# Optimization experiments

Hardware: AMD Instinct MI355X
Metric: run time of the kernel (lower is better)

Reference implementation:

```python
import jax, jax.numpy as jnp
import numpy as np

B, T, C, H = 128, 256, 256, 8
HS = C // H  # 32
EPS = 1e-5


def _layernorm(x, g, b):
    mu = jnp.mean(x, axis=-1, keepdims=True)
    var = jnp.mean(jnp.square(x - mu), axis=-1, keepdims=True)
    return g * (x - mu) / jnp.sqrt(var + EPS) + b


def setup_inputs() -> dict:
    key = jax.random.key(0)
    ks = jax.random.split(key, 12)
    s = 0.02
    return {
        "x": jax.random.normal(ks[0], (B, T, C), dtype=jnp.float32),
        "Wk": jax.random.normal(ks[1], (H, C, HS), dtype=jnp.float32) * s,
        "Wq": jax.random.normal(ks[2], (H, C, HS), dtype=jnp.float32) * s,
        "Wv": jax.random.normal(ks[3], (H, C, HS), dtype=jnp.float32) * s,
        "Wp": jax.random.normal(ks[4], (C, C), dtype=jnp.float32) * s,
        "bp": jnp.zeros((C,), dtype=jnp.float32),
        "W1": jax.random.normal(ks[5], (C, 4 * C), dtype=jnp.float32) * s,
        "b1": jnp.zeros((4 * C,), dtype=jnp.float32),
        "W2": jax.random.normal(ks[6], (4 * C, C), dtype=jnp.float32) * s,
        "b2": jnp.zeros((C,), dtype=jnp.float32),
        "g1": jnp.ones((C,), dtype=jnp.float32),
        "be1": jnp.zeros((C,), dtype=jnp.float32),
        "g2": jnp.ones((C,), dtype=jnp.float32),
        "be2": jnp.zeros((C,), dtype=jnp.float32),
    }


def reference(x, Wk, Wq, Wv, Wp, bp, W1, b1, W2, b2, g1, be1, g2, be2):
    Bx, Tx, Cx = x.shape
    # --- multi-head self-attention on ln1(x) ---
    h = _layernorm(x, g1, be1)
    k = jnp.einsum('btc,hcd->bhtd', h, Wk)
    q = jnp.einsum('btc,hcd->bhtd', h, Wq)
    v = jnp.einsum('btc,hcd->bhtd', h, Wv)
    # NOTE: source computes k @ q^T (transposed vs standard) and scales by C**-0.5
    scores = jnp.einsum('bhtd,bhsd->bhts', k, q) * (Cx ** -0.5)
    mask = jnp.tril(jnp.ones((Tx, Tx), dtype=bool))  # causal lower-triangular
    scores = jnp.where(mask, scores, -jnp.inf)
    w = jax.nn.softmax(scores, axis=-1)
    o = jnp.einsum('bhts,bhsd->bhtd', w, v)
    o = o.transpose(0, 2, 1, 3).reshape(Bx, Tx, Cx)  # concat heads
    x = x + (o @ Wp + bp)
    # --- feed-forward (swish) on ln2(x) ---
    h2 = _layernorm(x, g2, be2)
    f = h2 @ W1 + b1
    f = f * jax.nn.sigmoid(f)  # swish
    f = f @ W2 + b2
    return x + f
```

## Files before the change

kernel.cpp:

```cpp
#include <hip/hip_runtime.h>
#include <cstdint>

#define BB 128
#define TT 256
#define CC 256
#define HH 8
#define HSZ 32
#define NT (BB*TT)
#define CF (4*CC)
#define LN_EPS 1e-5f
#define SCALE 0.0625f

typedef __attribute__((ext_vector_type(8))) __bf16 bf16x8;
typedef __attribute__((ext_vector_type(4))) float f32x4;
typedef __attribute__((ext_vector_type(16))) float f32x16;
typedef __attribute__((ext_vector_type(2))) long i64x2;
typedef unsigned short u16;
typedef unsigned int u32;
typedef unsigned char u8;

__device__ __forceinline__ u16 f2bf(float f) {
  u32 u = __float_as_uint(f);
  u32 r = (u + 0x7fffu + ((u >> 16) & 1u)) >> 16;
  return (u16)r;
}
__device__ __forceinline__ u8 f2f8(float f) {
  return (u8)(__builtin_amdgcn_cvt_pk_fp8_f32(f, f, 0, false) & 0xff);
}
__device__ __forceinline__ u32 f2f8x4(float a, float b, float c, float d) {
  u32 pk = (u32)__builtin_amdgcn_cvt_pk_fp8_f32(a, b, 0, false);
  return (u32)__builtin_amdgcn_cvt_pk_fp8_f32(c, d, (int)pk, true);
}
__device__ __forceinline__ uint2 f2bfx4(float a, float b, float c, float d) {
  uint2 r;
  asm("v_cvt_pk_bf16_f32 %0, %1, %2" : "=v"(r.x) : "v"(a), "v"(b));
  asm("v_cvt_pk_bf16_f32 %0, %1, %2" : "=v"(r.y) : "v"(c), "v"(d));
  return r;
}
__device__ __forceinline__ int swz3i(int r) { return (r ^ (r >> 2)) & 3; }
__device__ __forceinline__ int pkrow(int row, int k) {
  int g = (k >> 4) & 3, h = (k >> 3) & 1, j = k & 7;
  int c = (h << 1) + (g >> 1);
  int cp = c ^ swz3i(row);
  return (k & ~63) + cp * 16 + ((g & 1) << 3) + j;
}

__device__ __forceinline__ void gload16(const void* g, void* l) {
  __builtin_amdgcn_global_load_lds(
      (const __attribute__((address_space(1))) u32*)(uintptr_t)g,
      (__attribute__((address_space(3))) u32*)(u32)(uintptr_t)l,
      16, 0, 0);
}

__device__ __forceinline__ void wait_vm0() {
  asm volatile("s_waitcnt vmcnt(0)" ::: "memory");
  __builtin_amdgcn_sched_barrier(0);
}
__device__ __forceinline__ void wait_vm4() {
  asm volatile("s_waitcnt vmcnt(4)" ::: "memory");
  __builtin_amdgcn_sched_barrier(0);
}
__device__ __forceinline__ void wait_vm8() {
  asm volatile("s_waitcnt vmcnt(8)" ::: "memory");
  __builtin_amdgcn_sched_barrier(0);
}
__device__ __forceinline__ void wait_vm4_lgkm0() {
  asm volatile("s_waitcnt vmcnt(4) lgkmcnt(0)" ::: "memory");
  __builtin_amdgcn_sched_barrier(0);
}
__device__ __forceinline__ void wait_vm0_lgkm0() {
  asm volatile("s_waitcnt vmcnt(0) lgkmcnt(0)" ::: "memory");
  __builtin_amdgcn_sched_barrier(0);
}
__device__ __forceinline__ void sbar() {
  __builtin_amdgcn_s_barrier();
  __builtin_amdgcn_sched_barrier(0);
}

__global__ __launch_bounds__(256) void conv_t(
    const float* __restrict__ Wk, const float* __restrict__ Wq,
    const float* __restrict__ Wv, const float* __restrict__ Wp,
    const float* __restrict__ W1, const float* __restrict__ W2,
    u8* __restrict__ WkqvT8, u8* __restrict__ WpT8,
    u8* __restrict__ W1T8, u8* __restrict__ W2T8) {
  __shared__ u8 ldsT[64][68];
  int bid = blockIdx.x, tid = threadIdx.x;
  int n0, k0, K;
  u8* dst;
  int mode;
  const float* src = nullptr;
  int sk = 0;
  if (bid < 48) {
    mode = 0; n0 = (bid >> 2) * 64; k0 = (bid & 3) * 64; K = 256; dst = WkqvT8;
  } else if (bid < 112) {
    int l = bid - 48;
    mode = 1; n0 = (l >> 2) * 64; k0 = (l & 3) * 64; K = 256; dst = W1T8;
    src = W1; sk = 1024;
  } else if (bid < 176) {
    int l = bid - 112;
    mode = 1; n0 = (l >> 4) * 64; k0 = (l & 15) * 64; K = 1024; dst = W2T8;
    src = W2; sk = 256;
  } else {
    int l = bid - 176;
    mode = 1; n0 = (l >> 2) * 64; k0 = (l & 3) * 64; K = 256; dst = WpT8;
    src = Wp; sk = 256;
  }
  int kr = tid >> 2;
  int nbase = (tid & 3) * 16;
#pragma unroll
  for (int u = 0; u < 4; ++u) {
    int nl = nbase + u * 4;
    int ng = n0 + nl;
    float4 v;
    if (mode == 0) {
      const float* W = (ng < 256) ? Wk : (ng < 512 ? Wq : Wv);
      int inner = ng & 255;
      v = *reinterpret_cast<const float4*>(
          &W[((inner >> 5) << 13) + (size_t)(k0 + kr) * 32 + (inner & 31)]);
    } else {
      v = *reinterpret_cast<const float4*>(
          &src[(size_t)(k0 + kr) * sk + ng]);
    }
    ldsT[nl + 0][kr] = f2f8(v.x);
    ldsT[nl + 1][kr] = f2f8(v.y);
    ldsT[nl + 2][kr] = f2f8(v.z);
    ldsT[nl + 3][kr] = f2f8(v.w);
  }
  __syncthreads();
  int nl = tid >> 2;
  int nglob = n0 + nl;
  int sz = swz3i(nglob);
  u8* drow = dst + (size_t)nglob * K + k0;
#pragma unroll
  for (int c4 = (tid & 3) * 4; c4 < (tid & 3) * 4 + 4; ++c4) {
    int q = c4 >> 1, s = c4 & 1;
    int kb = q * 8 + s * 4;
    u32 pk = (u32)ldsT[nl][kb] | ((u32)ldsT[nl][kb + 1] << 8) |
             ((u32)ldsT[nl][kb + 2] << 16) | ((u32)ldsT[nl][kb + 3] << 24);
    int g = (kb >> 4) & 3, h8 = (kb >> 3) & 1;
    int cp = ((h8 << 1) + (g >> 1)) ^ sz;
    *reinterpret_cast<u32*>(drow + cp * 16 + ((g & 1) << 3) + (kb & 7)) = pk;
  }
}

__global__ __launch_bounds__(256) void ln_kernel(const float* __restrict__ x,
                                                 const float* __restrict__ g,
                                                 const float* __restrict__ b,
                                                 u8* __restrict__ out) {
  int tid = threadIdx.x;
  int wid = tid >> 6, lane = tid & 63;
  int row = blockIdx.x * 4 + wid;
  const float4 v = reinterpret_cast<const float4*>(x + (size_t)row * CC)[lane];
  float s = v.x + v.y + v.z + v.w;
#pragma unroll
  for (int o = 32; o; o >>= 1) s += __shfl_xor(s, o, 64);
  float mu = s * (1.0f / CC);
  float dx = v.x - mu, dy = v.y - mu, dz = v.z - mu, dw = v.w - mu;
  float ss = dx * dx + dy * dy + dz * dz + dw * dw;
#pragma unroll
  for (int o = 32; o; o >>= 1) ss += __shfl_xor(ss, o, 64);
  float inv = rsqrtf(ss * (1.0f / CC) + LN_EPS);
  const float4 gv = reinterpret_cast<const float4*>(g)[lane];
  const float4 bv = reinterpret_cast<const float4*>(b)[lane];
  u32 pk = f2f8x4(gv.x * dx * inv + bv.x, gv.y * dy * inv + bv.y,
                  gv.z * dz * inv + bv.z, gv.w * dw * inv + bv.w);
  *reinterpret_cast<u32*>(out + (size_t)row * CC + pkrow(row, lane * 4)) = pk;
}

template <int EPI>
__device__ __forceinline__ void epi_store(f32x4 v, int m, int n,
                                          const float* bias,
                                          const float* resid, void* outp,
                                          int N) {
  size_t off = (size_t)m * N + n;
  if (EPI == 0) {
    u16 pk[4];
#pragma unroll
    for (int r = 0; r < 4; ++r) pk[r] = f2bf(v[r]);
    *reinterpret_cast<uint2*>(&((u16*)outp)[off]) = *reinterpret_cast<uint2*>(pk);
  } else if (EPI == 1) {
    const float4 bv = *reinterpret_cast<const float4*>(&bias[n]);
    const float4 rv = *reinterpret_cast<const float4*>(&resid[off]);
    float4 o;
    o.x = v[0] + bv.x + rv.x;
    o.y = v[1] + bv.y + rv.y;
    o.z = v[2] + bv.z + rv.z;
    o.w = v[3] + bv.w + rv.w;
    *reinterpret_cast<float4*>(&((float*)outp)[off]) = o;
  }
}

template <int NB, int EPI>
__global__ __launch_bounds__(512, 4) void panel_fused(
    const u8* __restrict__ Asrc, const u8* __restrict__ WT8,
    const float* __restrict__ bias, const float* __restrict__ resid,
    void* __restrict__ outp, int N,
    const float* __restrict__ gamma, const float* __restrict__ beta,
    u8* __restrict__ out8) {
  __shared__ u8 Bw[4][256][64];
  __shared__ float red[4][64][2];
  int tid = threadIdx.x;
  int w = tid >> 6, lane = tid & 63;
  int l32 = lane & 31, h = lane >> 5;
  int th = w >> 2, fq = w & 3;
  int m0 = blockIdx.x * 64;

#define STAGEP(nb)                                                            \
  {                                                                           \
    _Pragma("unroll") for (int it = 0; it < 8; ++it) {                        \
      int f = it * 512 + tid;                                                 \
      int kg = f >> 10, t = (f >> 2) & 255, c = f & 3;                        \
      gload16(WT8 + (size_t)((nb) * 256 + t) * 256 + kg * 64 + c * 16,        \
              &Bw[0][0][0] + f * 16);                                         \
    }                                                                         \
  }
  i64x2 aa[4][2];
  {
    int ar = th * 32 + l32;
    int az = swz3i(ar);
#pragma unroll
    for (int kg = 0; kg < 4; ++kg)
#pragma unroll
      for (int p = 0; p < 2; ++p)
        aa[kg][p] = *reinterpret_cast<const i64x2*>(
            Asrc + (size_t)(m0 + ar) * 256 + kg * 64 +
            ((((h << 1) + p) ^ az) << 4));
  }
  STAGEP(0);

#pragma unroll 1
  for (int nb = 0; nb < NB; ++nb) {
    if (nb == 0) wait_vm0(); else wait_vm8();
    sbar();
    f32x16 a1[2] = {};
#pragma unroll
    for (int kg = 0; kg < 4; ++kg) {
#pragma unroll
      for (int p = 0; p < 2; ++p) {
        i64x2 bB[2];
#pragma unroll
        for (int j = 0; j < 2; ++j) {
          int br = fq * 64 + j * 32 + l32, bz = swz3i(br);
          bB[j] = *reinterpret_cast<const i64x2*>(
              &Bw[kg][br][(((h << 1) + p) ^ bz) << 4]);
        }
#pragma unroll
        for (int j = 0; j < 2; ++j) {
          a1[j] = __builtin_amdgcn_mfma_f32_32x32x16_fp8_fp8(
              bB[j][0], aa[kg][p][0], a1[j], 0, 0, 0);
          a1[j] = __builtin_amdgcn_mfma_f32_32x32x16_fp8_fp8(
              bB[j][1], aa[kg][p][1], a1[j], 0, 0, 0);
        }
      }
    }
    sbar();
    if (nb < NB - 1) STAGEP(nb + 1);

    int m = m0 + th * 32 + l32;
    if (EPI == 2) {
      float s1 = 0.f, s2 = 0.f;
#pragma unroll
      for (int j = 0; j < 2; ++j) {
#pragma unroll
        for (int q = 0; q < 4; ++q) {
          int n = fq * 64 + j * 32 + q * 8 + h * 4;
          size_t off = (size_t)m * 256 + n;
          const float4 bv = *reinterpret_cast<const float4*>(&bias[n]);
          const float4 rv = *reinterpret_cast<const float4*>(&resid[off]);
          float4 o;
          o.x = a1[j][q * 4 + 0] + bv.x + rv.x;
          o.y = a1[j][q * 4 + 1] + bv.y + rv.y;
          o.z = a1[j][q * 4 + 2] + bv.z + rv.z;
          o.w = a1[j][q * 4 + 3] + bv.w + rv.w;
          *reinterpret_cast<float4*>(&((float*)outp)[off]) = o;
          a1[j][q * 4 + 0] = o.x; a1[j][q * 4 + 1] = o.y;
          a1[j][q * 4 + 2] = o.z; a1[j][q * 4 + 3] = o.w;
          s1 += (o.x + o.y) + (o.z + o.w);
          s2 += (o.x * o.x + o.y * o.y) + (o.z * o.z + o.w * o.w);
        }
      }
      s1 += __shfl_xor(s1, 32, 64);
      s2 += __shfl_xor(s2, 32, 64);
      if (h == 0) { red[fq][th * 32 + l32][0] = s1; red[fq][th * 32 + l32][1] = s2; }
      sbar();
      int tl = th * 32 + l32;
      float S1 = (red[0][tl][0] + red[1][tl][0]) + (red[2][tl][0] + red[3][tl][0]);
      float S2 = (red[0][tl][1] + red[1][tl][1]) + (red[2][tl][1] + red[3][tl][1]);
      float mu = S1 * (1.0f / 256.0f);
      float inv = rsqrtf(S2 * (1.0f / 256.0f) - mu * mu + LN_EPS);
#pragma unroll
      for (int j = 0; j < 2; ++j) {
#pragma unroll
        for (int q = 0; q < 4; ++q) {
          int n = fq * 64 + j * 32 + q * 8 + h * 4;
          const float4 gv = *reinterpret_cast<const float4*>(&gamma[n]);
          const float4 bb = *reinterpret_cast<const float4*>(&beta[n]);
          u32 pk = f2f8x4(gv.x * (a1[j][q * 4 + 0] - mu) * inv + bb.x,
                          gv.y * (a1[j][q * 4 + 1] - mu) * inv + bb.y,
                          gv.z * (a1[j][q * 4 + 2] - mu) * inv + bb.z,
                          gv.w * (a1[j][q * 4 + 3] - mu) * inv + bb.w);
          *reinterpret_cast<u32*>(out8 + (size_t)m * 256 + pkrow(m, n)) = pk;
        }
      }
    } else {
#pragma unroll
      for (int j = 0; j < 2; ++j) {
#pragma unroll
        for (int q = 0; q < 4; ++q) {
          int n = nb * 256 + fq * 64 + j * 32 + q * 8 + h * 4;
          f32x4 v = {a1[j][q * 4 + 0], a1[j][q * 4 + 1],
                     a1[j][q * 4 + 2], a1[j][q * 4 + 3]};
          epi_store<EPI>(v, m, n, bias, resid, outp, N);
        }
      }
    }
  }
#undef STAGEP
}

__global__ __launch_bounds__(512, 4) void ffn_fused(
    const u8* __restrict__ hb, const u8* __restrict__ W1T8,
    const u8* __restrict__ W2T8, const float* __restrict__ b1,
    const float* __restrict__ b2, const float* __restrict__ x2,
    float* __restrict__ outp) {
  __shared__ u8 Bw1[4][128][64];
  __shared__ u8 Bw2[2][256][64];
  __shared__ u8 Ff[2][64][64];
  __shared__ float b1l[1024];
  int tid = threadIdx.x;
  int w = tid >> 6, lane = tid & 63;
  int l32 = lane & 31, h = lane >> 5;
  int th = w >> 2, fq = w & 3;
  int m0 = blockIdx.x * 64;

#define STAGE_W1(nb)                                                          \
  {                                                                           \
    _Pragma("unroll") for (int it = 0; it < 4; ++it) {                        \
      int f = it * 512 + tid;                                                 \
      int kg = f >> 9, t = (f >> 2) & 127, c = f & 3;                         \
      gload16(W1T8 + (size_t)((nb) * 128 + t) * 256 + kg * 64 + c * 16,       \
              &Bw1[0][0][0] + f * 16);                                        \
    }                                                                         \
  }
#define STAGE_W2(nb)                                                          \
  {                                                                           \
    _Pragma("unroll") for (int it = 0; it < 4; ++it) {                        \
      int f = it * 512 + tid;                                                 \
      int kg2 = f >> 10, o = (f >> 2) & 255, c = f & 3;                       \
      gload16(W2T8 + (size_t)o * 1024 + (nb) * 128 + kg2 * 64 + c * 16,       \
              &Bw2[0][0][0] + f * 16);                                        \
    }                                                                         \
  }
  i64x2 aa[4][2];
  {
    int ar = th * 32 + l32;
    int az = swz3i(ar);
#pragma unroll
    for (int kg = 0; kg < 4; ++kg)
#pragma unroll
      for (int p = 0; p < 2; ++p)
        aa[kg][p] = *reinterpret_cast<const i64x2*>(
            hb + (size_t)(m0 + ar) * 256 + kg * 64 +
            ((((h << 1) + p) ^ az) << 4));
  }
  if (w < 4) gload16(b1 + (size_t)(w * 256 + lane * 4), b1l + w * 256 + lane * 4);
  STAGE_W1(0);
  STAGE_W2(0);

  f32x16 acc2[2] = {};
#pragma unroll 1
  for (int nb = 0; nb < 8; ++nb) {
    wait_vm4();
    sbar();
    f32x16 a1 = {};
#pragma unroll
    for (int kg = 0; kg < 4; ++kg) {
      int br = fq * 32 + l32, bz = swz3i(br);
#pragma unroll
      for (int p = 0; p < 2; ++p) {
        i64x2 bB = *reinterpret_cast<const i64x2*>(
            &Bw1[kg][br][(((h << 1) + p) ^ bz) << 4]);
        a1 = __builtin_amdgcn_mfma_f32_32x32x16_fp8_fp8(
            bB[0], aa[kg][p][0], a1, 0, 0, 0);
        a1 = __builtin_amdgcn_mfma_f32_32x32x16_fp8_fp8(
            bB[1], aa[kg][p][1], a1, 0, 0, 0);
      }
    }
    sbar();
    if (nb < 7) STAGE_W1(nb + 1);
    int kg2w = fq >> 1;
    {
      int t = th * 32 + l32;
      int tz = swz3i(t);
#pragma unroll
      for (int q = 0; q < 4; ++q) {
        int g = (fq & 1) * 2 + (q >> 1);
        int hh = q & 1;
        int c = (hh << 1) + (g >> 1);
        const float4 bv = *reinterpret_cast<const float4*>(
            &b1l[nb * 128 + fq * 32 + q * 8 + h * 4]);
        float bf[4] = {bv.x, bv.y, bv.z, bv.w};
        float sv[4];
#pragma unroll
        for (int r = 0; r < 4; ++r) {
          float fv = a1[q * 4 + r] + bf[r];
          float e = __builtin_amdgcn_exp2f(fv * -1.44269504f);
          sv[r] = fv * __builtin_amdgcn_rcpf(1.0f + e);
        }
        *reinterpret_cast<u32*>(
            &Ff[kg2w][t][((c ^ tz) << 4) + ((g & 1) << 3) + h * 4]) =
            f2f8x4(sv[0], sv[1], sv[2], sv[3]);
      }
    }
    if (nb < 7) wait_vm4_lgkm0();
    else        wait_vm0_lgkm0();
    sbar();
#pragma unroll
    for (int kg2 = 0; kg2 < 2; ++kg2)
#pragma unroll
      for (int p = 0; p < 2; ++p) {
        int ar2 = th * 32 + l32;
        i64x2 fa = *reinterpret_cast<const i64x2*>(
            &Ff[kg2][ar2][(((h << 1) + p) ^ swz3i(ar2)) << 4]);
        i64x2 bb2[2];
#pragma unroll
        for (int j = 0; j < 2; ++j) {
          int br = fq * 64 + j * 32 + l32;
          bb2[j] = *reinterpret_cast<const i64x2*>(
              &Bw2[kg2][br][(((h << 1) + p) ^ swz3i(br)) << 4]);
        }
#pragma unroll
        for (int j = 0; j < 2; ++j) {
          acc2[j] = __builtin_amdgcn_mfma_f32_32x32x16_fp8_fp8(
              bb2[j][0], fa[0], acc2[j], 0, 0, 0);
          acc2[j] = __builtin_amdgcn_mfma_f32_32x32x16_fp8_fp8(
              bb2[j][1], fa[1], acc2[j], 0, 0, 0);
        }
      }
    sbar();
    if (nb < 7) STAGE_W2(nb + 1);
  }
#undef STAGE_W1
#undef STAGE_W2
  int m = m0 + th * 32 + l32;
#pragma unroll
  for (int j = 0; j < 2; ++j) {
#pragma unroll
    for (int q = 0; q < 4; ++q) {
      int n = fq * 64 + j * 32 + q * 8 + h * 4;
      f32x4 v = {acc2[j][q * 4 + 0], acc2[j][q * 4 + 1],
                 acc2[j][q * 4 + 2], acc2[j][q * 4 + 3]};
      epi_store<1>(v, m, n, b2, x2, outp, CC);
    }
  }
}

__global__ __launch_bounds__(512) void attn_kernel(const u16* __restrict__ kqv,
                                                   u8* __restrict__ o8) {
  __shared__ u16 q_lds[256 * 32];
  __shared__ u16 vT[32 * 256];
  __shared__ u16 pT[8 * 16 * 64];
  int bh = blockIdx.x;
  int b = bh >> 3, h = bh & 7;
  int tid = threadIdx.x, wid = tid >> 6, lane = tid & 63;
  int l16 = lane & 15, lh = lane >> 4;
  const size_t rowbase = (size_t)b * TT * 768;
  {
    int sr = tid >> 2, c = tid & 3;
#pragma unroll
    for (int s = sr; s < 256; s += 128) {
      uint4 qv = *reinterpret_cast<const uint4*>(
          &kqv[rowbase + (size_t)s * 768 + 256 + h * 32 + c * 8]);
      *reinterpret_cast<uint4*>((char*)q_lds + ((s * 64 + c * 16) ^ ((s & 7) << 4))) = qv;
      u16 tmp[8];
      *reinterpret_cast<uint4*>(tmp) = *reinterpret_cast<const uint4*>(
          &kqv[rowbase + (size_t)s * 768 + 512 + h * 32 + c * 8]);
#pragma unroll
      for (int dd = 0; dd < 8; ++dd) {
        int e = dd ^ c;
        int d = c * 8 + e;
        vT[d * 256 + (((s >> 3) ^ (d & 7)) << 3) + (s & 7)] = tmp[e];
      }
    }
  }
  __syncthreads();
  u16* pw = &pT[wid * 16 * 64];
  const float C1 = 0.09016844f;
#pragma unroll
  for (int jj = 0; jj < 2; ++jj) {
    int ti = jj * 8 + wid;
    int t16 = ti * 16;
    int stmax = ti >> 2;
    bf16x8 kb = *reinterpret_cast<const bf16x8*>(
        &kqv[rowbase + (size_t)(t16 + l16) * 768 + h * 32 + lh * 8]);
    float m2 = -3e38f, lsum = 0.f;
    f32x4 oacc[2] = {};
    for (int st = 0; st <= stmax; ++st) {
      int s0 = st << 6;
      float v[4][4];
      float pm[4];
#pragma unroll
      for (int sj = 0; sj < 4; ++sj) {
        int srow = s0 + sj * 16 + l16;
        bf16x8 qa = *reinterpret_cast<const bf16x8*>(
            (char*)q_lds + ((srow * 64 + lh * 16) ^ ((srow & 7) << 4)));
        f32x4 z = {0.f, 0.f, 0.f, 0.f};
        f32x4 sc = __builtin_amdgcn_mfma_f32_16x16x32_bf16(qa, kb, z, 0, 0, 0);
#pragma unroll
        for (int r = 0; r < 4; ++r) {
          float val = sc[r];
          if (st == stmax) {
            if (sj * 16 + lh * 4 + r > (ti & 3) * 16 + l16) val = -3e38f;
          }
          v[sj][r] = val;
        }
        pm[sj] = fmaxf(fmaxf(v[sj][0], v[sj][1]), fmaxf(v[sj][2], v[sj][3]));
      }
      float mx = fmaxf(fmaxf(pm[0], pm[1]), fmaxf(pm[2], pm[3]));
      mx = fmaxf(mx, __shfl_xor(mx, 16, 64));
      mx = fmaxf(mx, __shfl_xor(mx, 32, 64));
      float mxs = mx * C1;
      if (!__all(mxs <= m2 + 8.0f)) {
        float mn = fmaxf(m2, mxs);
        float alpha = exp2f(m2 - mn);
        m2 = mn;
        lsum *= alpha;
#pragma unroll
        for (int r = 0; r < 4; ++r) {
          float a = __shfl(alpha, (lane & 48) | (lh * 4 + r), 64);
          oacc[0][r] *= a;
          oacc[1][r] *= a;
        }
      }
#pragma unroll
      for (int sj = 0; sj < 4; ++sj) {
        float p0 = exp2f(__builtin_fmaf(v[sj][0], C1, -m2));
        float p1 = exp2f(__builtin_fmaf(v[sj][1], C1, -m2));
        float p2 = exp2f(__builtin_fmaf(v[sj][2], C1, -m2));
        float p3 = exp2f(__builtin_fmaf(v[sj][3], C1, -m2));
        lsum += (p0 + p1) + (p2 + p3);
        uint2 pkv = f2bfx4(p0, p1, p2, p3);
        *reinterpret_cast<uint2*>(
            (char*)pw + ((l16 * 128 + sj * 32 + lh * 8) ^ ((l16 & 7) << 4))) = pkv;
      }
#pragma unroll
      for (int ks = 0; ks < 2; ++ks) {
        bf16x8 pa = *reinterpret_cast<const bf16x8*>(
            (char*)pw + ((l16 * 128 + ks * 64 + lh * 16) ^ ((l16 & 7) << 4)));
#pragma unroll
        for (int nI = 0; nI < 2; ++nI) {
          int d = nI * 16 + l16;
          int sch = ((s0 + ks * 32 + lh * 8) >> 3) ^ (d & 7);
          bf16x8 vb = *reinterpret_cast<const bf16x8*>(&vT[d * 256 + (sch << 3)]);
          oacc[nI] = __builtin_amdgcn_mfma_f32_16x16x32_bf16(pa, vb, oacc[nI], 0, 0, 0);
        }
      }
    }
    lsum += __shfl_xor(lsum, 16, 64);
    lsum += __shfl_xor(lsum, 32, 64);
#pragma unroll
    for (int r = 0; r < 4; ++r) {
      float ls = __shfl(lsum, (lane & 48) | (lh * 4 + r), 64);
      float inv = 1.0f / ls;
      int t = t16 + lh * 4 + r;
      size_t rb = (size_t)(b * TT + t) * CC;
#pragma unroll
      for (int nI = 0; nI < 2; ++nI) {
        int c = h * HSZ + nI * 16 + l16;
        o8[rb + pkrow(t, c)] = f2f8(oacc[nI][r] * inv);
      }
    }
  }
}

extern "C" void kernel_launch(void* const* d_in, const int* in_sizes, int n_in,
                              void* d_out, int out_size, void* d_ws, size_t ws_size,
                              hipStream_t stream) {
  const float* x   = (const float*)d_in[0];
  const float* Wk  = (const float*)d_in[1];
  const float* Wq  = (const float*)d_in[2];
  const float* Wv  = (const float*)d_in[3];
  const float* Wp  = (const float*)d_in[4];
  const float* bp  = (const float*)d_in[5];
  const float* W1  = (const float*)d_in[6];
  const float* b1  = (const float*)d_in[7];
  const float* W2  = (const float*)d_in[8];
  const float* b2  = (const float*)d_in[9];
  const float* g1  = (const float*)d_in[10];
  const float* be1 = (const float*)d_in[11];
  const float* g2  = (const float*)d_in[12];
  const float* be2 = (const float*)d_in[13];

  char* ws = (char*)d_ws;
  u16* kqv = (u16*)(ws + 0);
  u8*  o8  = (u8*)(ws + 50331648);
  float* x2 = (float*)(ws + 67108864);
  u8*  hb  = (u8*)(ws + 100663296);
  char* wb = ws + 117440512;
  u8*  WkqvT8 = (u8*)(wb);
  u8*  WpT8   = (u8*)(wb + 196608);
  u8*  W1T8   = (u8*)(wb + 196608 + 65536);
  u8*  W2T8   = (u8*)(wb + 196608 + 65536 + 262144);

  conv_t<<<192, 256, 0, stream>>>(Wk, Wq, Wv, Wp, W1, W2,
                                  WkqvT8, WpT8, W1T8, W2T8);
  ln_kernel<<<NT / 4, 256, 0, stream>>>(x, g1, be1, hb);
  panel_fused<3, 0><<<NT / 64, 512, 0, stream>>>(
      hb, WkqvT8, nullptr, nullptr, kqv, 768, nullptr, nullptr, nullptr);
  attn_kernel<<<BB * HH, 512, 0, stream>>>(kqv, o8);
  panel_fused<1, 2><<<NT / 64, 512, 0, stream>>>(
      o8, WpT8, bp, x, x2, 256, g2, be2, hb);
  ffn_fused<<<NT / 64, 512, 0, stream>>>(hb, W1T8, W2T8, b1, b2, x2, (float*)d_out);
}
```

Before: 136.4 us.

## Merge weight conversion with LN1, shrink attention blocks, delay W1 staging in FFN

The weight transpose/convert kernel and the first layernorm kernel become one launch, with extra blocks doing the layernorm, which removes one kernel launch boundary. The attention kernel now runs 256 threads instead of 512, each wave covering 4 query tiles with a balanced causal workload and half the P scratch in LDS. In the FFN kernel, staging of the next W1 tile moves after the full wait and barrier, so it no longer overlaps with the swish epilogue. This may reduce prefetch overlap, and attention has fewer waves per block.

```diff
diff --git a/kernel.cpp b/kernel.cpp
--- a/kernel.cpp
+++ b/kernel.cpp
@@ -64,10 +64,6 @@
   asm volatile("s_waitcnt vmcnt(8)" ::: "memory");
   __builtin_amdgcn_sched_barrier(0);
 }
-__device__ __forceinline__ void wait_vm4_lgkm0() {
-  asm volatile("s_waitcnt vmcnt(4) lgkmcnt(0)" ::: "memory");
-  __builtin_amdgcn_sched_barrier(0);
-}
 __device__ __forceinline__ void wait_vm0_lgkm0() {
   asm volatile("s_waitcnt vmcnt(0) lgkmcnt(0)" ::: "memory");
   __builtin_amdgcn_sched_barrier(0);
@@ -77,14 +73,36 @@
   __builtin_amdgcn_sched_barrier(0);
 }
 
-__global__ __launch_bounds__(256) void conv_t(
+__global__ __launch_bounds__(256) void conv_ln(
     const float* __restrict__ Wk, const float* __restrict__ Wq,
     const float* __restrict__ Wv, const float* __restrict__ Wp,
     const float* __restrict__ W1, const float* __restrict__ W2,
     u8* __restrict__ WkqvT8, u8* __restrict__ WpT8,
-    u8* __restrict__ W1T8, u8* __restrict__ W2T8) {
+    u8* __restrict__ W1T8, u8* __restrict__ W2T8,
+    const float* __restrict__ x, const float* __restrict__ g1,
+    const float* __restrict__ be1, u8* __restrict__ hb) {
   __shared__ u8 ldsT[64][68];
   int bid = blockIdx.x, tid = threadIdx.x;
+  if (bid >= 192) {
+    int wid = tid >> 6, lane = tid & 63;
+    int row = (bid - 192) * 4 + wid;
+    const float4 v = reinterpret_cast<const float4*>(x + (size_t)row * CC)[lane];
+    float s = v.x + v.y + v.z + v.w;
+#pragma unroll
+    for (int o = 32; o; o >>= 1) s += __shfl_xor(s, o, 64);
+    float mu = s * (1.0f / CC);
+    float dx = v.x - mu, dy = v.y - mu, dz = v.z - mu, dw = v.w - mu;
+    float ss = dx * dx + dy * dy + dz * dz + dw * dw;
+#pragma unroll
+    for (int o = 32; o; o >>= 1) ss += __shfl_xor(ss, o, 64);
+    float inv = rsqrtf(ss * (1.0f / CC) + LN_EPS);
+    const float4 gv = reinterpret_cast<const float4*>(g1)[lane];
+    const float4 bv = reinterpret_cast<const float4*>(be1)[lane];
+    u32 pk = f2f8x4(gv.x * dx * inv + bv.x, gv.y * dy * inv + bv.y,
+                    gv.z * dz * inv + bv.z, gv.w * dw * inv + bv.w);
+    *reinterpret_cast<u32*>(hb + (size_t)row * CC + pkrow(row, lane * 4)) = pk;
+    return;
+  }
   int n0, k0, K;
   u8* dst;
   int mode;
@@ -143,30 +161,6 @@
   }
 }
 
-__global__ __launch_bounds__(256) void ln_kernel(const float* __restrict__ x,
-                                                 const float* __restrict__ g,
-                                                 const float* __restrict__ b,
-                                                 u8* __restrict__ out) {
-  int tid = threadIdx.x;
-  int wid = tid >> 6, lane = tid & 63;
-  int row = blockIdx.x * 4 + wid;
-  const float4 v = reinterpret_cast<const float4*>(x + (size_t)row * CC)[lane];
-  float s = v.x + v.y + v.z + v.w;
-#pragma unroll
-  for (int o = 32; o; o >>= 1) s += __shfl_xor(s, o, 64);
-  float mu = s * (1.0f / CC);
-  float dx = v.x - mu, dy = v.y - mu, dz = v.z - mu, dw = v.w - mu;
-  float ss = dx * dx + dy * dy + dz * dz + dw * dw;
-#pragma unroll
-  for (int o = 32; o; o >>= 1) ss += __shfl_xor(ss, o, 64);
-  float inv = rsqrtf(ss * (1.0f / CC) + LN_EPS);
-  const float4 gv = reinterpret_cast<const float4*>(g)[lane];
-  const float4 bv = reinterpret_cast<const float4*>(b)[lane];
-  u32 pk = f2f8x4(gv.x * dx * inv + bv.x, gv.y * dy * inv + bv.y,
-                  gv.z * dz * inv + bv.z, gv.w * dw * inv + bv.w);
-  *reinterpret_cast<u32*>(out + (size_t)row * CC + pkrow(row, lane * 4)) = pk;
-}
-
 template <int EPI>
 __device__ __forceinline__ void epi_store(f32x4 v, int m, int n,
                                           const float* bias,
@@ -386,8 +380,6 @@
             bB[1], aa[kg][p][1], a1, 0, 0, 0);
       }
     }
-    sbar();
-    if (nb < 7) STAGE_W1(nb + 1);
     int kg2w = fq >> 1;
     {
       int t = th * 32 + l32;
@@ -412,9 +404,9 @@
             f2f8x4(sv[0], sv[1], sv[2], sv[3]);
       }
     }
-    if (nb < 7) wait_vm4_lgkm0();
-    else        wait_vm0_lgkm0();
+    wait_vm0_lgkm0();
     sbar();
+    if (nb < 7) STAGE_W1(nb + 1);
 #pragma unroll
     for (int kg2 = 0; kg2 < 2; ++kg2)
 #pragma unroll
@@ -455,11 +447,11 @@
   }
 }
 
-__global__ __launch_bounds__(512) void attn_kernel(const u16* __restrict__ kqv,
+__global__ __launch_bounds__(256) void attn_kernel(const u16* __restrict__ kqv,
                                                    u8* __restrict__ o8) {
   __shared__ u16 q_lds[256 * 32];
   __shared__ u16 vT[32 * 256];
-  __shared__ u16 pT[8 * 16 * 64];
+  __shared__ u16 pT[4 * 16 * 64];
   int bh = blockIdx.x;
   int b = bh >> 3, h = bh & 7;
   int tid = threadIdx.x, wid = tid >> 6, lane = tid & 63;
@@ -467,8 +459,7 @@
   const size_t rowbase = (size_t)b * TT * 768;
   {
     int sr = tid >> 2, c = tid & 3;
-#pragma unroll
-    for (int s = sr; s < 256; s += 128) {
+    for (int s = sr; s < 256; s += 64) {
       uint4 qv = *reinterpret_cast<const uint4*>(
           &kqv[rowbase + (size_t)s * 768 + 256 + h * 32 + c * 8]);
       *reinterpret_cast<uint4*>((char*)q_lds + ((s * 64 + c * 16) ^ ((s & 7) << 4))) = qv;
@@ -486,16 +477,13 @@
   __syncthreads();
   u16* pw = &pT[wid * 16 * 64];
   const float C1 = 0.09016844f;
-#pragma unroll
-  for (int jj = 0; jj < 2; ++jj) {
-    int ti = jj * 8 + wid;
-    int t16 = ti * 16;
-    int stmax = ti >> 2;
+  for (int j = 0; j < 4; ++j) {
+    int t16 = (j * 4 + wid) * 16;
     bf16x8 kb = *reinterpret_cast<const bf16x8*>(
         &kqv[rowbase + (size_t)(t16 + l16) * 768 + h * 32 + lh * 8]);
     float m2 = -3e38f, lsum = 0.f;
     f32x4 oacc[2] = {};
-    for (int st = 0; st <= stmax; ++st) {
+    for (int st = 0; st <= j; ++st) {
       int s0 = st << 6;
       float v[4][4];
       float pm[4];
@@ -509,8 +497,8 @@
 #pragma unroll
         for (int r = 0; r < 4; ++r) {
           float val = sc[r];
-          if (st == stmax) {
-            if (sj * 16 + lh * 4 + r > (ti & 3) * 16 + l16) val = -3e38f;
+          if (st == j) {
+            if (sj * 16 + lh * 4 + r > wid * 16 + l16) val = -3e38f;
           }
           v[sj][r] = val;
         }
@@ -602,12 +590,12 @@
   u8*  W1T8   = (u8*)(wb + 196608 + 65536);
   u8*  W2T8   = (u8*)(wb + 196608 + 65536 + 262144);
 
-  conv_t<<<192, 256, 0, stream>>>(Wk, Wq, Wv, Wp, W1, W2,
-                                  WkqvT8, WpT8, W1T8, W2T8);
-  ln_kernel<<<NT / 4, 256, 0, stream>>>(x, g1, be1, hb);
+  conv_ln<<<192 + NT / 4, 256, 0, stream>>>(Wk, Wq, Wv, Wp, W1, W2,
+                                            WkqvT8, WpT8, W1T8, W2T8,
+                                            x, g1, be1, hb);
   panel_fused<3, 0><<<NT / 64, 512, 0, stream>>>(
       hb, WkqvT8, nullptr, nullptr, kqv, 768, nullptr, nullptr, nullptr);
-  attn_kernel<<<BB * HH, 512, 0, stream>>>(kqv, o8);
+  attn_kernel<<<BB * HH, 256, 0, stream>>>(kqv, o8);
   panel_fused<1, 2><<<NT / 64, 512, 0, stream>>>(
       o8, WpT8, bp, x, x2, 256, g2, be2, hb);
   ffn_fused<<<NT / 64, 512, 0, stream>>>(hb, W1T8, W2T8, b1, b2, x2, (float*)d_out);
```

New measurement: 135.3 us. No clear change (-0.8%).
